# Optimization experiments

Measured on AMD Instinct MI355X. Metric: run time of the kernel, lower is better.

The kernel has to match this reference:

```python
import jax, jax.numpy as jnp
import numpy as np

N = 100000
E = 1600000
F = 64
THETA = (0.6, -0.4, 0.3, -0.2, 0.1)  # k = 5 polynomial coefficients


def setup_inputs() -> dict:
    key = jax.random.key(0)
    kx, ke = jax.random.split(key)
    x = jax.random.normal(kx, (N, F), dtype=jnp.float32)
    edge_index = jax.random.randint(ke, (2, E), 0, N, dtype=jnp.int64)
    return {"x": x, "edge_index": edge_index}


def _l_sym_mul(feat, src, dst, deg_inv_sqrt, n):
    # L_sym * feat = feat - D^{-1/2} A D^{-1/2} feat
    src_norm = feat[src] * deg_inv_sqrt[src]            # [E, F] gather + scale
    agg = jax.ops.segment_sum(src_norm, dst, num_segments=n)  # scatter-add to dst
    return feat - deg_inv_sqrt * agg


def reference(x, edge_index):
    src, dst = edge_index[0], edge_index[1]
    n = x.shape[0]
    # in-degree from dst, clamp to >= 1, D^{-1/2} as [N, 1]
    deg = jax.ops.segment_sum(jnp.ones((src.shape[0],), dtype=x.dtype), dst,
                              num_segments=n)
    deg = jnp.maximum(deg, 1.0)[:, None]
    deg_inv_sqrt = deg ** -0.5

    h_acc = THETA[0] * x
    feat = x
    for k in range(1, len(THETA)):
        feat = _l_sym_mul(feat, src, dst, deg_inv_sqrt, n)
        h_acc = h_acc + THETA[k] * feat
    return h_acc
```

## Files before the change

kernel.cpp:

```cpp
#include <hip/hip_runtime.h>
#include <hip/hip_fp16.h>


constexpr int kF = 64;
constexpr int BSHIFT = 8;
constexpr int NB = 1 << BSHIFT;
constexpr int TILEA = 4096;
constexpr int KMAX = 512;

typedef unsigned nv4u __attribute__((ext_vector_type(4)));
typedef float    nv4f __attribute__((ext_vector_type(4)));

static __device__ __forceinline__ float hlo(unsigned u) {
    return __half2float(__ushort_as_half((unsigned short)(u & 0xffffu)));
}
static __device__ __forceinline__ float hhi(unsigned u) {
    return __half2float(__ushort_as_half((unsigned short)(u >> 16)));
}
static __device__ __forceinline__ unsigned pack2h(float a, float b) {
    return (unsigned)__half_as_ushort(__float2half_rn(a)) |
           ((unsigned)__half_as_ushort(__float2half_rn(b)) << 16);
}
static __device__ __forceinline__ unsigned padd2(unsigned a, unsigned b) {
    __half2 ha = *reinterpret_cast<__half2*>(&a);
    __half2 hb = *reinterpret_cast<__half2*>(&b);
    __half2 hc = __hadd2(ha, hb);
    return *reinterpret_cast<unsigned*>(&hc);
}

__global__ void k_binA(const int* __restrict__ src, const int* __restrict__ dst,
                       unsigned* __restrict__ pairs, int* __restrict__ gcursor,
                       int E, int K, int cap) {
    __shared__ unsigned stage[TILEA];
    __shared__ unsigned short stageB[TILEA];
    __shared__ int hist[KMAX];
    __shared__ int lb[KMAX];
    __shared__ int gb[KMAX];
    const int tid = threadIdx.x;
    const long long tb = (long long)blockIdx.x * TILEA;
    const int tcount = (int)min((long long)TILEA, (long long)E - tb);

    hist[tid] = 0;
    __syncthreads();
    int dc[8], sc[8];
    #pragma unroll
    for (int k = 0; k < 8; ++k) {
        int i = tid + k * 512;
        if (i < tcount) {
            dc[k] = dst[tb + i];
            sc[k] = src[tb + i];
            atomicAdd(&hist[dc[k] >> BSHIFT], 1);
        } else {
            dc[k] = -1;
        }
    }
    __syncthreads();
    const int cnt = hist[tid];
    lb[tid] = cnt;
    __syncthreads();
    for (int o = 1; o < KMAX; o <<= 1) {
        int t = (tid >= o) ? lb[tid - o] : 0;
        __syncthreads();
        lb[tid] += t;
        __syncthreads();
    }
    const int excl = lb[tid] - cnt;
    __syncthreads();
    lb[tid] = excl;
    gb[tid] = (tid < K && cnt > 0) ? atomicAdd(&gcursor[tid], cnt) : 0;
    hist[tid] = excl;
    __syncthreads();
    #pragma unroll
    for (int k = 0; k < 8; ++k) {
        if (dc[k] >= 0) {
            int d = dc[k];
            int b = d >> BSHIFT;
            int pos = atomicAdd(&hist[b], 1);
            stage[pos]  = ((unsigned)(d & (NB - 1)) << 23) | (unsigned)sc[k];
            stageB[pos] = (unsigned short)b;
        }
    }
    __syncthreads();
    for (int j = tid; j < tcount; j += 512) {
        int b = stageB[j];
        pairs[(size_t)b * cap + gb[b] + (j - lb[b])] = stage[j];
    }
}

__global__ void k_binB(const unsigned* __restrict__ pairs, const int* __restrict__ gcursor,
                       int* __restrict__ rp, float* __restrict__ dinv2,
                       float* __restrict__ rdeg, int* __restrict__ csr,
                       int* __restrict__ csr0,
                       const float4* __restrict__ x4,
                       uint4* __restrict__ xb4, uint4* __restrict__ g0,
                       int N, int E, int K, int cap) {
    __shared__ int gsc[KMAX];
    __shared__ int cnt[NB];
    __shared__ int stmp[NB];
    __shared__ int cur[NB];
    __shared__ float sdinv[NB];
    const int b = blockIdx.x;
    const int tid = threadIdx.x;

    if (b == 0 && tid < 8)
        g0[((size_t)N << 3) + tid] = make_uint4(0, 0, 0, 0);

    int gv = (tid < K) ? gcursor[tid] : 0;
    gsc[tid] = gv;
    __syncthreads();
    for (int o = 1; o < KMAX; o <<= 1) {
        int t = (tid >= o) ? gsc[tid - o] : 0;
        __syncthreads();
        gsc[tid] += t;
        __syncthreads();
    }
    const int ecnt = gcursor[b];
    const int base = gsc[b] - ecnt;
    const unsigned* bp = pairs + (size_t)b * cap;

    if (tid < NB) cnt[tid] = 0;
    __syncthreads();
    for (int i = tid; i < ecnt; i += 512)
        atomicAdd(&cnt[bp[i] >> 23], 1);
    __syncthreads();
    int v = (tid < NB) ? cnt[tid] : 0;
    if (tid < NB) stmp[tid] = v;
    __syncthreads();
    for (int o = 1; o < NB; o <<= 1) {
        int t = (tid >= o && tid < NB) ? stmp[tid - o] : 0;
        __syncthreads();
        if (tid < NB) stmp[tid] += t;
        __syncthreads();
    }
    int node = (b << BSHIFT) + tid;
    if (tid < NB) {
        int abs0 = base + stmp[tid] - v;
        cur[tid] = abs0;
        float d = fmaxf((float)v, 1.0f);
        sdinv[tid] = rsqrtf(d);
        if (node < N) {
            rp[node] = abs0;
            dinv2[node] = 1.0f / d;
            rdeg[node]  = sqrtf(d);
        }
    }
    if (b == K - 1 && tid == 0) rp[N] = E;
    __syncthreads();
    for (int i = tid; i < ecnt; i += 512) {
        unsigned p = bp[i];
        int pos = atomicAdd(&cur[p >> 23], 1);
        csr[pos] = (int)(p & 0x7FFFFFu);
    }
    __syncthreads();
    if (tid < NB && node < N) {
        int abs0 = base + stmp[tid] - v;
        int4 q0, q1;
        q0.x = (0 < v) ? csr[abs0 + 0] : N;
        q0.y = (1 < v) ? csr[abs0 + 1] : N;
        q0.z = (2 < v) ? csr[abs0 + 2] : N;
        q0.w = (3 < v) ? csr[abs0 + 3] : N;
        q1.x = (4 < v) ? csr[abs0 + 4] : N;
        q1.y = (5 < v) ? csr[abs0 + 5] : N;
        q1.z = (6 < v) ? csr[abs0 + 6] : N;
        q1.w = (7 < v) ? csr[abs0 + 7] : N;
        *(int4*)(csr0 + ((size_t)node << 3))     = q0;
        *(int4*)(csr0 + ((size_t)node << 3) + 4) = q1;
    }
    const int nbase = b << BSHIFT;
    const int qmax = min(NB, N - nbase) << 3;
    uint4* g0p = g0 + ((size_t)nbase << 3);
    for (int q = tid; q < qmax; q += 512) {
        int gq = ((nbase + (q >> 3)) << 3) + (q & 7);
        float4 a = x4[2 * gq];
        float4 bb = x4[2 * gq + 1];
        uint4 xo;
        xo.x = pack2h(a.x, a.y);
        xo.y = pack2h(a.z, a.w);
        xo.z = pack2h(bb.x, bb.y);
        xo.w = pack2h(bb.z, bb.w);
        xb4[gq] = xo;
        float di = sdinv[q >> 3];
        uint4 go;
        go.x = pack2h(di * a.x, di * a.y);
        go.y = pack2h(di * a.z, di * a.w);
        go.z = pack2h(di * bb.x, di * bb.y);
        go.w = pack2h(di * bb.z, di * bb.w);
        g0p[q] = go;
    }
}

template <bool LAST>
__global__ void k_gather(const int* __restrict__ rp, const int* __restrict__ csr,
                         const int* __restrict__ csr0,
                         const unsigned short* __restrict__ gin,
                         const float* __restrict__ dinv2,
                         unsigned short* __restrict__ gout,
                         const unsigned short* __restrict__ xb,
                         const unsigned short* __restrict__ g1t,
                         const unsigned short* __restrict__ g2t,
                         const float* __restrict__ rdeg,
                         float* __restrict__ h, int n,
                         float t0, float t1, float t2, float t3, float t4) {
    if (!LAST && blockIdx.x == 0 && threadIdx.x < 8)
        *(((uint4*)(gout + ((size_t)n << 6))) + threadIdx.x) = make_uint4(0, 0, 0, 0);

    int wid = (blockIdx.x * blockDim.x + threadIdx.x) >> 6;
    int lane = threadIdx.x & 63;
    int half = lane >> 5;
    int r = (lane >> 3) & 3;
    int c = lane & 7;
    int node = wid * 2 + half;
    if (wid * 2 >= n) return;
    bool valid = node < n;

    int s1 = n, s2 = n;
    if (valid) {
        s1 = csr0[((size_t)node << 3) + r];
        s2 = csr0[((size_t)node << 3) + r + 4];
    }
    int beg = valid ? rp[node] : 0;
    int end = valid ? rp[node + 1] : 0;

    const bool ep = (r == 0) && valid;
    size_t off = ((size_t)node << 6) + (c << 3);
    uint4 rr = make_uint4(0, 0, 0, 0);
    float d2 = 0.f, rd = 0.f;
    nv4u xv = {0u, 0u, 0u, 0u}, aa = {0u, 0u, 0u, 0u}, bb = {0u, 0u, 0u, 0u};
    if (ep) {
        rr = *(const uint4*)(gin + off);
        d2 = dinv2[node];
        if (LAST) {
            xv = __builtin_nontemporal_load((const nv4u*)(xb + off));
            aa = __builtin_nontemporal_load((const nv4u*)(g1t + off));
            bb = __builtin_nontemporal_load((const nv4u*)(g2t + off));
            rd = rdeg[node];
        }
    }

    int len = end - beg;
    int olen = __shfl_xor(len, 32, 64);
    int mlen = (len > olen) ? len : olen;

    unsigned acc[4] = {0u, 0u, 0u, 0u};

    uint4 rc1 = *(const uint4*)(gin + ((size_t)s1 << 6) + (c << 3));
    uint4 rc2 = *(const uint4*)(gin + ((size_t)s2 << 6) + (c << 3));
    int sn1 = n, sn2 = n;
    {
        int j1b = beg + 8 + r, j2b = j1b + 4;
        bool vb = 8 < mlen;
        bool b1 = vb && (j1b < end), b2 = vb && (j2b < end);
        sn1 = csr[b1 ? j1b : 0]; sn1 = b1 ? sn1 : n;
        sn2 = csr[b2 ? j2b : 0]; sn2 = b2 ? sn2 : n;
    }
    for (int i = 0; i < mlen; i += 8) {
        uint4 rn1 = *(const uint4*)(gin + ((size_t)sn1 << 6) + (c << 3));
        uint4 rn2 = *(const uint4*)(gin + ((size_t)sn2 << 6) + (c << 3));
        int j1n = beg + i + 16 + r, j2n = j1n + 4;
        bool vn = (i + 16) < mlen;
        bool t1c = vn && (j1n < end), t2c = vn && (j2n < end);
        int st1 = csr[t1c ? j1n : 0]; st1 = t1c ? st1 : n;
        int st2 = csr[t2c ? j2n : 0]; st2 = t2c ? st2 : n;
        acc[0] = padd2(acc[0], rc1.x); acc[1] = padd2(acc[1], rc1.y);
        acc[2] = padd2(acc[2], rc1.z); acc[3] = padd2(acc[3], rc1.w);
        acc[0] = padd2(acc[0], rc2.x); acc[1] = padd2(acc[1], rc2.y);
        acc[2] = padd2(acc[2], rc2.z); acc[3] = padd2(acc[3], rc2.w);
        rc1 = rn1; rc2 = rn2;
        sn1 = st1; sn2 = st2;
    }
    #pragma unroll
    for (int m = 8; m <= 16; m <<= 1) {
        #pragma unroll
        for (int i = 0; i < 4; ++i)
            acc[i] = padd2(acc[i], __shfl_xor(acc[i], m, 64));
    }

    if (ep) {
        float v[8];
        v[0] = hlo(rr.x) - d2 * hlo(acc[0]); v[1] = hhi(rr.x) - d2 * hhi(acc[0]);
        v[2] = hlo(rr.y) - d2 * hlo(acc[1]); v[3] = hhi(rr.y) - d2 * hhi(acc[1]);
        v[4] = hlo(rr.z) - d2 * hlo(acc[2]); v[5] = hhi(rr.z) - d2 * hhi(acc[2]);
        v[6] = hlo(rr.w) - d2 * hlo(acc[3]); v[7] = hhi(rr.w) - d2 * hhi(acc[3]);
        if (!LAST) {
            nv4u o;
            o.x = pack2h(v[0], v[1]);
            o.y = pack2h(v[2], v[3]);
            o.z = pack2h(v[4], v[5]);
            o.w = pack2h(v[6], v[7]);
            __builtin_nontemporal_store(o, (nv4u*)(gout + off));
        } else {
            float s1f = rd * t1, s2f = rd * t2, s3f = rd * t3, s4f = rd * t4;
            nv4f h0, h1;
            h0.x = t0 * hlo(xv.x) + s1f * hlo(aa.x) + s2f * hlo(bb.x) + s3f * hlo(rr.x) + s4f * v[0];
            h0.y = t0 * hhi(xv.x) + s1f * hhi(aa.x) + s2f * hhi(bb.x) + s3f * hhi(rr.x) + s4f * v[1];
            h0.z = t0 * hlo(xv.y) + s1f * hlo(aa.y) + s2f * hlo(bb.y) + s3f * hlo(rr.y) + s4f * v[2];
            h0.w = t0 * hhi(xv.y) + s1f * hhi(aa.y) + s2f * hhi(bb.y) + s3f * hhi(rr.y) + s4f * v[3];
            h1.x = t0 * hlo(xv.z) + s1f * hlo(aa.z) + s2f * hlo(bb.z) + s3f * hlo(rr.z) + s4f * v[4];
            h1.y = t0 * hhi(xv.z) + s1f * hhi(aa.z) + s2f * hhi(bb.z) + s3f * hhi(rr.z) + s4f * v[5];
            h1.z = t0 * hlo(xv.w) + s1f * hlo(aa.w) + s2f * hlo(bb.w) + s3f * hlo(rr.w) + s4f * v[6];
            h1.w = t0 * hhi(xv.w) + s1f * hhi(aa.w) + s2f * hhi(bb.w) + s3f * hhi(rr.w) + s4f * v[7];
            __builtin_nontemporal_store(h0, (nv4f*)(h + off));
            __builtin_nontemporal_store(h1, (nv4f*)(h + off + 4));
        }
    }
}

extern "C" void kernel_launch(void* const* d_in, const int* in_sizes, int n_in,
                              void* d_out, int out_size, void* d_ws, size_t ws_size,
                              hipStream_t stream) {
    const float* x  = (const float*)d_in[0];
    const int*   ei = (const int*)d_in[1];
    const int N = in_sizes[0] / kF;
    const int E = in_sizes[1] / 2;
    const int* src = ei;
    const int* dst = ei + E;
    float* h = (float*)d_out;

    const int K = (N + NB - 1) >> BSHIFT;
    const int cap = 2 * ((E + K - 1) / K);

    char* ws = (char*)d_ws;
    size_t off = 0;
    auto carve = [&](size_t bytes) {
        void* p = ws + off;
        off = (off + bytes + 511) & ~(size_t)511;
        return p;
    };
    size_t gbytes = (size_t)(N + 1) * kF * 2;
    int*            gcursor = (int*)carve((size_t)KMAX * 4);
    int*            rp      = (int*)carve((size_t)(N + 1) * 4);
    float*          dinv2   = (float*)carve((size_t)N * 4);
    float*          rdeg    = (float*)carve((size_t)N * 4);
    int*            csr     = (int*)carve((size_t)E * 4);
    int*            csr0    = (int*)carve((size_t)N * 8 * 4);
    unsigned short* xb      = (unsigned short*)carve((size_t)N * kF * 2);
    unsigned short* g0      = (unsigned short*)carve(gbytes);
    size_t pbytes = (size_t)K * cap * 4;
    unsigned short* g1      = (unsigned short*)carve(gbytes > pbytes ? gbytes : pbytes);
    unsigned short* g2      = (unsigned short*)carve(gbytes);
    unsigned short* g3      = (unsigned short*)carve(gbytes);
    unsigned*       pairs   = (unsigned*)g1;

    const float theta[5] = {0.6f, -0.4f, 0.3f, -0.2f, 0.1f};

    hipMemsetAsync(gcursor, 0, (size_t)KMAX * 4, stream);
    k_binA<<<(E + TILEA - 1) / TILEA, 512, 0, stream>>>(src, dst, pairs, gcursor,
                                                        E, K, cap);
    k_binB<<<K, 512, 0, stream>>>(pairs, gcursor, rp, dinv2, rdeg, csr, csr0,
                                  (const float4*)x, (uint4*)xb, (uint4*)g0,
                                  N, E, K, cap);

    const int nwaves = (N + 1) / 2;
    const int gblocks = (nwaves + 3) / 4;
    k_gather<false><<<gblocks, 256, 0, stream>>>(rp, csr, csr0, g0, dinv2, g1,
                                                 nullptr, nullptr, nullptr, nullptr,
                                                 nullptr, N, 0, 0, 0, 0, 0);
    k_gather<false><<<gblocks, 256, 0, stream>>>(rp, csr, csr0, g1, dinv2, g2,
                                                 nullptr, nullptr, nullptr, nullptr,
                                                 nullptr, N, 0, 0, 0, 0, 0);
    k_gather<false><<<gblocks, 256, 0, stream>>>(rp, csr, csr0, g2, dinv2, g3,
                                                 nullptr, nullptr, nullptr, nullptr,
                                                 nullptr, N, 0, 0, 0, 0, 0);
    k_gather<true><<<gblocks, 256, 0, stream>>>(rp, csr, csr0, g3, dinv2, nullptr,
                                                xb, g1, g2, rdeg, h, N,
                                                theta[0], theta[1], theta[2],
                                                theta[3], theta[4]);
}
```

Baseline: 235.9 us.

## Fuse four gather passes into one persistent cooperative kernel with grid syncs

Replaces the four separate k_gather launches with a single cooperative kernel of 1024 blocks. Each block loops over node pairs in a grid-stride fashion and separates the Laplacian hops with grid.sync() plus threadfence. This removes per-launch overhead and the inter-kernel gaps. In exchange it adds grid-wide barriers, limits the grid to the co-resident blocks (cooperative launch can fail if 1024x256 blocks cannot all be resident), and gives less latency hiding than a full-size grid.

New measurement: 911.0 us. 3.86x slower.

```diff
diff --git a/kernel.cpp b/kernel.cpp
--- a/kernel.cpp
+++ b/kernel.cpp
@@ -1,5 +1,8 @@
 #include <hip/hip_runtime.h>
 #include <hip/hip_fp16.h>
+#include <hip/hip_cooperative_groups.h>
+
+namespace cg = cooperative_groups;
 
 
 constexpr int kF = 64;
@@ -7,6 +10,7 @@
 constexpr int NB = 1 << BSHIFT;
 constexpr int TILEA = 4096;
 constexpr int KMAX = 512;
+constexpr int GBLK = 1024;
 
 typedef unsigned nv4u __attribute__((ext_vector_type(4)));
 typedef float    nv4f __attribute__((ext_vector_type(4)));
@@ -190,22 +194,19 @@
 }
 
 template <bool LAST>
-__global__ void k_gather(const int* __restrict__ rp, const int* __restrict__ csr,
-                         const int* __restrict__ csr0,
-                         const unsigned short* __restrict__ gin,
-                         const float* __restrict__ dinv2,
-                         unsigned short* __restrict__ gout,
-                         const unsigned short* __restrict__ xb,
-                         const unsigned short* __restrict__ g1t,
-                         const unsigned short* __restrict__ g2t,
-                         const float* __restrict__ rdeg,
-                         float* __restrict__ h, int n,
-                         float t0, float t1, float t2, float t3, float t4) {
-    if (!LAST && blockIdx.x == 0 && threadIdx.x < 8)
-        *(((uint4*)(gout + ((size_t)n << 6))) + threadIdx.x) = make_uint4(0, 0, 0, 0);
-
-    int wid = (blockIdx.x * blockDim.x + threadIdx.x) >> 6;
-    int lane = threadIdx.x & 63;
+static __device__ __forceinline__ void gather_pair(
+        int wid, int lane,
+        const int* __restrict__ rp, const int* __restrict__ csr,
+        const int* __restrict__ csr0,
+        const unsigned short* __restrict__ gin,
+        const float* __restrict__ dinv2,
+        unsigned short* __restrict__ gout,
+        const unsigned short* __restrict__ xb,
+        const unsigned short* __restrict__ g1t,
+        const unsigned short* __restrict__ g2t,
+        const float* __restrict__ rdeg,
+        float* __restrict__ h, int n,
+        float t0, float t1, float t2, float t3, float t4) {
     int half = lane >> 5;
     int r = (lane >> 3) & 3;
     int c = lane & 7;
@@ -305,6 +306,50 @@
     }
 }
 
+__global__ void k_gather4(const int* __restrict__ rp, const int* __restrict__ csr,
+                          const int* __restrict__ csr0,
+                          unsigned short* __restrict__ g0,
+                          unsigned short* __restrict__ g1,
+                          unsigned short* __restrict__ g2,
+                          unsigned short* __restrict__ g3,
+                          const float* __restrict__ dinv2,
+                          const unsigned short* __restrict__ xb,
+                          const float* __restrict__ rdeg,
+                          float* __restrict__ h, int n, int npairs,
+                          float t0, float t1, float t2, float t3, float t4) {
+    cg::grid_group grid = cg::this_grid();
+    const int gwave  = (blockIdx.x * blockDim.x + threadIdx.x) >> 6;
+    const int nwaves = (gridDim.x * blockDim.x) >> 6;
+    const int lane   = threadIdx.x & 63;
+
+    if (blockIdx.x == 0 && threadIdx.x < 24) {
+        unsigned short* t = (threadIdx.x < 8) ? g1 : (threadIdx.x < 16) ? g2 : g3;
+        *(((uint4*)(t + ((size_t)n << 6))) + (threadIdx.x & 7)) = make_uint4(0, 0, 0, 0);
+    }
+
+    for (int p = gwave; p < npairs; p += nwaves)
+        gather_pair<false>(p, lane, rp, csr, csr0, g0, dinv2, g1,
+                           nullptr, nullptr, nullptr, nullptr, nullptr,
+                           n, 0, 0, 0, 0, 0);
+    __threadfence();
+    grid.sync();
+    for (int p = gwave; p < npairs; p += nwaves)
+        gather_pair<false>(p, lane, rp, csr, csr0, g1, dinv2, g2,
+                           nullptr, nullptr, nullptr, nullptr, nullptr,
+                           n, 0, 0, 0, 0, 0);
+    __threadfence();
+    grid.sync();
+    for (int p = gwave; p < npairs; p += nwaves)
+        gather_pair<false>(p, lane, rp, csr, csr0, g2, dinv2, g3,
+                           nullptr, nullptr, nullptr, nullptr, nullptr,
+                           n, 0, 0, 0, 0, 0);
+    __threadfence();
+    grid.sync();
+    for (int p = gwave; p < npairs; p += nwaves)
+        gather_pair<true>(p, lane, rp, csr, csr0, g3, dinv2, nullptr,
+                          xb, g1, g2, rdeg, h, n, t0, t1, t2, t3, t4);
+}
+
 extern "C" void kernel_launch(void* const* d_in, const int* in_sizes, int n_in,
                               void* d_out, int out_size, void* d_ws, size_t ws_size,
                               hipStream_t stream) {
@@ -350,19 +395,15 @@
                                   (const float4*)x, (uint4*)xb, (uint4*)g0,
                                   N, E, K, cap);
 
-    const int nwaves = (N + 1) / 2;
-    const int gblocks = (nwaves + 3) / 4;
-    k_gather<false><<<gblocks, 256, 0, stream>>>(rp, csr, csr0, g0, dinv2, g1,
-                                                 nullptr, nullptr, nullptr, nullptr,
-                                                 nullptr, N, 0, 0, 0, 0, 0);
-    k_gather<false><<<gblocks, 256, 0, stream>>>(rp, csr, csr0, g1, dinv2, g2,
-                                                 nullptr, nullptr, nullptr, nullptr,
-                                                 nullptr, N, 0, 0, 0, 0, 0);
-    k_gather<false><<<gblocks, 256, 0, stream>>>(rp, csr, csr0, g2, dinv2, g3,
-                                                 nullptr, nullptr, nullptr, nullptr,
-                                                 nullptr, N, 0, 0, 0, 0, 0);
-    k_gather<true><<<gblocks, 256, 0, stream>>>(rp, csr, csr0, g3, dinv2, nullptr,
-                                                xb, g1, g2, rdeg, h, N,
-                                                theta[0], theta[1], theta[2],
-                                                theta[3], theta[4]);
-}
+    int npairs = (N + 1) / 2;
+    float t0 = theta[0], t1 = theta[1], t2 = theta[2], t3 = theta[3], t4 = theta[4];
+    void* args[] = {
+        (void*)&rp, (void*)&csr, (void*)&csr0,
+        (void*)&g0, (void*)&g1, (void*)&g2, (void*)&g3,
+        (void*)&dinv2, (void*)&xb, (void*)&rdeg, (void*)&h,
+        (void*)&N, (void*)&npairs,
+        (void*)&t0, (void*)&t1, (void*)&t2, (void*)&t3, (void*)&t4
+    };
+    hipLaunchCooperativeKernel((void*)k_gather4, dim3(GBLK), dim3(256),
+                               args, 0, stream);
+}
```
